# Kernel tuning notes

Measured on AMD Instinct MI355X. Metric: run time of the kernel, lower is better.

The kernel has to match this reference:

```python
import jax, jax.numpy as jnp
import numpy as np

HEADS = 8
DIM_HEAD = 32
SCALE = DIM_HEAD ** (-0.5)


def setup_inputs() -> dict:
    key = jax.random.key(0)
    k1, k2, k3, k4 = jax.random.split(key, 4)
    x = jax.random.normal(k1, (16, 256, 64, 64), dtype=jnp.float32)
    # conv 1x1 weights stored as [out_ch, in_ch]
    w_qkv = jax.random.normal(k2, (3 * HEADS * DIM_HEAD, 256), dtype=jnp.float32) * 0.05
    w_out = jax.random.normal(k3, (256, HEADS * DIM_HEAD), dtype=jnp.float32) * 0.05
    b_out = jax.random.normal(k4, (256,), dtype=jnp.float32) * 0.05
    return {"x": x, "w_qkv": w_qkv, "w_out": w_out, "b_out": b_out}


def reference(x, w_qkv, w_out, b_out):
    b, c, h, w = x.shape
    n = h * w
    # 1x1 conv (no bias) == channel matmul
    qkv = jnp.einsum('bchw,oc->bohw', x, w_qkv)            # [b, 3*H*D, h, w]
    qkv = qkv.reshape(b, 3, HEADS, DIM_HEAD, n)            # chunk then 'b (h c) xy'
    q, k, v = qkv[:, 0], qkv[:, 1], qkv[:, 2]              # [b, H, D, n]
    q = jax.nn.softmax(q, axis=-2) * SCALE                 # softmax over channel dim d
    k = jax.nn.softmax(k, axis=-1)                         # softmax over spatial n
    context = jnp.einsum('bhdn,bhen->bhde', k, v)          # [b, H, D, D]
    out = jnp.einsum('bhde,bhdn->bhen', context, q)        # [b, H, D, n]
    out = out.reshape(b, HEADS * DIM_HEAD, h, w)
    # 1x1 conv with bias
    return jnp.einsum('bchw,oc->bohw', out, w_out) + b_out[None, :, None, None]
```

## Files before the change

### kernel.cpp

```cpp
#include <hip/hip_runtime.h>
#include <cstddef>
#include <cstdint>

#define NN 4096
#define CIN 256
#define CQKV 768
#define NBATCH 16
#define KSPLIT 4
#define QSCALE 0.17677669529663687f

typedef short s16x8 __attribute__((ext_vector_type(8)));
typedef float f32x4 __attribute__((ext_vector_type(4)));

__device__ __forceinline__ float bf2f(unsigned short u) {
    unsigned int x = ((unsigned int)u) << 16;
    return __builtin_bit_cast(float, x);
}
__device__ __forceinline__ unsigned short f2bf(float f) {
    unsigned int u = __builtin_bit_cast(unsigned int, f);
    return (unsigned short)((u + 0x7fffu + ((u >> 16) & 1u)) >> 16);
}
__device__ __forceinline__ void glds16(const void* gsrc, void* lds) {
    __builtin_amdgcn_global_load_lds(
        (const __attribute__((address_space(1))) unsigned int*)gsrc,
        (__attribute__((address_space(3))) unsigned int*)lds,
        16, 0, 0);
}

__device__ __forceinline__ void gemm_core(const unsigned short* __restrict__ Ab,
                                          const unsigned short* __restrict__ Bb,
                                          int m0, int n0, char* smem,
                                          f32x4 (&acc)[4][4])
{
    const int t = threadIdx.x;
    const int lane = t & 63, w = t >> 6;
    const int lr = lane & 15, lq = lane >> 4;
    const int wr = (w >> 1) * 64, wc = (w & 1) * 64;
    const int srow = t >> 3;
    const int schunk = (t & 7) ^ (srow & 7);
    const int wq = w << 10;
    const int xr = lr & 7;

    char* A0 = smem;          char* B0 = smem + 16384;
    char* A1 = smem + 32768;  char* B1 = smem + 49152;

#define STG(bufA, bufB, k0)                                                     \
    { _Pragma("unroll") for (int i = 0; i < 4; ++i)                             \
        glds16(Ab + (size_t)(m0 + i*32 + srow)*256 + (k0) + schunk*8,           \
               (bufA) + i*4096 + wq);                                           \
      _Pragma("unroll") for (int i = 0; i < 4; ++i)                             \
        glds16(Bb + (size_t)(n0 + i*32 + srow)*256 + (k0) + schunk*8,           \
               (bufB) + i*4096 + wq); }

#define CMP(bufA, bufB)                                                         \
    { s16x8 af[4][2], bfr[4][2];                                                \
      _Pragma("unroll") for (int m = 0; m < 4; ++m) {                           \
        const char* rp = (bufA) + (wr + m*16 + lr)*128;                         \
        af[m][0] = *(const s16x8*)(rp + (((0*4 + lq) ^ xr) << 4));              \
        af[m][1] = *(const s16x8*)(rp + (((1*4 + lq) ^ xr) << 4)); }            \
      _Pragma("unroll") for (int n = 0; n < 4; ++n) {                           \
        const char* rp = (bufB) + (wc + n*16 + lr)*128;                         \
        bfr[n][0] = *(const s16x8*)(rp + (((0*4 + lq) ^ xr) << 4));             \
        bfr[n][1] = *(const s16x8*)(rp + (((1*4 + lq) ^ xr) << 4)); }           \
      _Pragma("unroll") for (int m = 0; m < 4; ++m)                             \
      _Pragma("unroll") for (int n = 0; n < 4; ++n) {                           \
        acc[m][n] = __builtin_amdgcn_mfma_f32_16x16x32_bf16(af[m][0], bfr[n][0], acc[m][n], 0, 0, 0); \
        acc[m][n] = __builtin_amdgcn_mfma_f32_16x16x32_bf16(af[m][1], bfr[n][1], acc[m][n], 0, 0, 0); }}

    STG(A0, B0, 0);
    __syncthreads();
    STG(A1, B1, 64);
    CMP(A0, B0);
    __syncthreads();
    STG(A0, B0, 128);
    CMP(A1, B1);
    __syncthreads();
    STG(A1, B1, 192);
    CMP(A0, B0);
    __syncthreads();
    CMP(A1, B1);
#undef STG
#undef CMP
}

__global__ __launch_bounds__(256, 2)
void gemm_qkv(const unsigned short* __restrict__ wb,
              const unsigned short* __restrict__ xT,
              unsigned short* __restrict__ qkv,
              unsigned short* __restrict__ qT)
{
    __shared__ __align__(16) char smem[65536];
    const int bz = blockIdx.z;
    const int m0 = blockIdx.y * 128, n0 = blockIdx.x * 128;
    const unsigned short* Bb = xT + (size_t)bz * NN * 256;

    f32x4 acc[4][4] = {};
    gemm_core(wb, Bb, m0, n0, smem, acc);

    const int t = threadIdx.x;
    const int lane = t & 63, w = t >> 6;
    const int lr = lane & 15, lq = lane >> 4;
    const int wr = (w >> 1) * 64, wc = (w & 1) * 64;

    if (m0 < 256) {
        __syncthreads();
        unsigned short (*qs)[136] = (unsigned short (*)[136])smem;
#pragma unroll
        for (int n = 0; n < 4; ++n) {
            const int col = wc + n * 16 + lr;
#pragma unroll
            for (int hp = 0; hp < 2; ++hp) {
                float mx = -1e30f;
#pragma unroll
                for (int u = 0; u < 2; ++u)
#pragma unroll
                    for (int r = 0; r < 4; ++r)
                        mx = fmaxf(mx, acc[hp * 2 + u][n][r]);
                mx = fmaxf(mx, __shfl_xor(mx, 16));
                mx = fmaxf(mx, __shfl_xor(mx, 32));
                float er[2][4];
                float s = 0.f;
#pragma unroll
                for (int u = 0; u < 2; ++u)
#pragma unroll
                    for (int r = 0; r < 4; ++r) {
                        er[u][r] = __expf(acc[hp * 2 + u][n][r] - mx);
                        s += er[u][r];
                    }
                s += __shfl_xor(s, 16);
                s += __shfl_xor(s, 32);
                const float inv = QSCALE / s;
#pragma unroll
                for (int u = 0; u < 2; ++u) {
                    ushort4 pk;
                    pk.x = f2bf(er[u][0] * inv);
                    pk.y = f2bf(er[u][1] * inv);
                    pk.z = f2bf(er[u][2] * inv);
                    pk.w = f2bf(er[u][3] * inv);
                    *(ushort4*)&qs[col][wr + (hp * 2 + u) * 16 + lq * 4] = pk;
                }
            }
        }
        __syncthreads();
        const int nl = t >> 1, half = t & 1;
        const unsigned short* src = &qs[nl][half * 64];
        unsigned short* dst = qT + ((size_t)bz * NN + n0 + nl) * 256 + m0 + half * 64;
#pragma unroll
        for (int i = 0; i < 8; ++i)
            *(s16x8*)(dst + i * 8) = *(const s16x8*)(src + i * 8);
    } else {
        unsigned short* Yb = qkv + (size_t)bz * CQKV * NN;
#pragma unroll
        for (int m = 0; m < 4; ++m)
#pragma unroll
            for (int r = 0; r < 4; ++r) {
                const int row = m0 + wr + m * 16 + lq * 4 + r;
#pragma unroll
                for (int n = 0; n < 4; ++n)
                    Yb[(size_t)row * NN + n0 + wc + n * 16 + lr] = f2bf(acc[m][n][r]);
            }
    }
}

__global__ __launch_bounds__(256, 2)
void gemm_out(const unsigned short* __restrict__ Mmat,
              const unsigned short* __restrict__ qT,
              float* __restrict__ out, const float* __restrict__ bias)
{
    __shared__ __align__(16) char smem[65536];
    const int bz = blockIdx.z;
    const int m0 = blockIdx.y * 128, n0 = blockIdx.x * 128;
    const unsigned short* Ab = Mmat + (size_t)bz * 256 * 256;
    const unsigned short* Bb = qT + (size_t)bz * NN * 256;

    f32x4 acc[4][4] = {};
    gemm_core(Ab, Bb, m0, n0, smem, acc);

    const int t = threadIdx.x;
    const int lane = t & 63, w = t >> 6;
    const int lr = lane & 15, lq = lane >> 4;
    const int wr = (w >> 1) * 64, wc = (w & 1) * 64;

    float* Yb = out + (size_t)bz * CIN * NN;
#pragma unroll
    for (int m = 0; m < 4; ++m)
#pragma unroll
        for (int r = 0; r < 4; ++r) {
            const int row = m0 + wr + m * 16 + lq * 4 + r;
            const float bv = bias[row];
#pragma unroll
            for (int n = 0; n < 4; ++n)
                Yb[(size_t)row * NN + n0 + wc + n * 16 + lr] = acc[m][n][r] + bv;
        }
}

__global__ __launch_bounds__(256)
void xpose(const float* __restrict__ x, unsigned short* __restrict__ xT)
{
    const int b = blockIdx.z;
    const int n0 = blockIdx.x * 64, c0 = blockIdx.y * 64;
    __shared__ float xs[64][65];
    const int t = threadIdx.x;
    const float* xb = x + (size_t)b * CIN * NN;
#pragma unroll
    for (int p = 0; p < 4; ++p) {
        const int row = p * 16 + (t >> 4);
        const int col = (t & 15) * 4;
        const float4 v = *reinterpret_cast<const float4*>(
            &xb[(size_t)(c0 + row) * NN + n0 + col]);
        xs[col + 0][row] = v.x; xs[col + 1][row] = v.y;
        xs[col + 2][row] = v.z; xs[col + 3][row] = v.w;
    }
    __syncthreads();
    const int n = t >> 2, cch = (t & 3) * 16;
    unsigned short arr[16];
#pragma unroll
    for (int e = 0; e < 16; ++e) arr[e] = f2bf(xs[n][cch + e]);
    unsigned short* dst = xT + ((size_t)b * NN + n0 + n) * 256 + c0 + cch;
    *reinterpret_cast<s16x8*>(&dst[0]) = *reinterpret_cast<s16x8*>(&arr[0]);
    *reinterpret_cast<s16x8*>(&dst[8]) = *reinterpret_cast<s16x8*>(&arr[8]);
}

__global__ __launch_bounds__(256)
void wcvt(const float* __restrict__ w, unsigned short* __restrict__ wb)
{
    const int i = (blockIdx.x * 256 + threadIdx.x) * 4;
    const float4 v = *reinterpret_cast<const float4*>(&w[i]);
    unsigned short a[4] = { f2bf(v.x), f2bf(v.y), f2bf(v.z), f2bf(v.w) };
    *reinterpret_cast<ushort2*>(&wb[i])     = *reinterpret_cast<ushort2*>(&a[0]);
    *reinterpret_cast<ushort2*>(&wb[i + 2]) = *reinterpret_cast<ushort2*>(&a[2]);
}

__global__ __launch_bounds__(256)
void kv_context(const unsigned short* __restrict__ qkv,
                float* __restrict__ ctx_part, float* __restrict__ z_part)
{
    const int bh = blockIdx.x;
    const int sp = blockIdx.y;
    const int b = bh >> 3, h = bh & 7;
    const unsigned short* kb = qkv + ((size_t)b * CQKV + 256 + h * 32) * NN;
    const unsigned short* vb = qkv + ((size_t)b * CQKV + 512 + h * 32) * NN;
    const int c0 = sp * (NN / KSPLIT);

    __shared__ float ek[64][36];
    __shared__ float vv[64][36];

    const int t = threadIdx.x;
    const int lane = t & 63;
    const int w = t >> 6;

    float zloc[8];
#pragma unroll
    for (int p = 0; p < 8; ++p) zloc[p] = 0.f;

    const int d0 = (lane >> 3) * 4;
    const int e0 = (lane & 7) * 4;
    float acc[4][4];
#pragma unroll
    for (int i = 0; i < 4; ++i)
#pragma unroll
        for (int j = 0; j < 4; ++j) acc[i][j] = 0.f;

    for (int cc = 0; cc < NN / KSPLIT; cc += 64) {
#pragma unroll
        for (int p = 0; p < 8; ++p) {
            const int d = w + 4 * p;
            const float kvv = bf2f(kb[(size_t)d * NN + c0 + cc + lane]);
            const float e = __expf(kvv);
            zloc[p] += e;
            ek[lane][d] = e;
            vv[lane][d] = bf2f(vb[(size_t)d * NN + c0 + cc + lane]);
        }
        __syncthreads();
#pragma unroll
        for (int ci = 0; ci < 16; ++ci) {
            const int c = w + 4 * ci;
            float ea[4], va[4];
            *reinterpret_cast<float4*>(ea) = *reinterpret_cast<const float4*>(&ek[c][d0]);
            *reinterpret_cast<float4*>(va) = *reinterpret_cast<const float4*>(&vv[c][e0]);
#pragma unroll
            for (int i = 0; i < 4; ++i)
#pragma unroll
                for (int j = 0; j < 4; ++j)
                    acc[i][j] = fmaf(ea[i], va[j], acc[i][j]);
        }
        __syncthreads();
    }

    float* dst = ctx_part + (((size_t)bh * KSPLIT + sp) * 4 + w) * 1024 + lane * 16;
#pragma unroll
    for (int i = 0; i < 4; ++i) {
        float4 v;
        v.x = acc[i][0]; v.y = acc[i][1]; v.z = acc[i][2]; v.w = acc[i][3];
        *reinterpret_cast<float4*>(&dst[i * 4]) = v;
    }
#pragma unroll
    for (int p = 0; p < 8; ++p) {
        float z = zloc[p];
#pragma unroll
        for (int off = 32; off >= 1; off >>= 1) z += __shfl_xor(z, off);
        if (lane == 0) z_part[((size_t)bh * KSPLIT + sp) * 32 + (w + 4 * p)] = z;
    }
}

__global__ __launch_bounds__(256)
void make_m(const float* __restrict__ ctx_part, const float* __restrict__ z_part,
            const float* __restrict__ w_out, unsigned short* __restrict__ Mmat)
{
    const int h = blockIdx.x;
    const int b = blockIdx.y;
    const int bh = b * 8 + h;
    const int t = threadIdx.x;

    __shared__ float ctx[32][33];
    __shared__ float zinv[32];

    for (int lin = t; lin < 1024; lin += 256) {
        const int g = lin >> 4, i = (lin >> 2) & 3, j = lin & 3;
        const int d = ((g >> 3) << 2) + i;
        const int e = ((g & 7) << 2) + j;
        float s = 0.f;
#pragma unroll
        for (int p = 0; p < 16; ++p)
            s += ctx_part[((size_t)bh * 16 + p) * 1024 + lin];
        ctx[d][e] = s;
    }
    if (t < 32) {
        float z = 0.f;
#pragma unroll
        for (int sp = 0; sp < KSPLIT; ++sp)
            z += z_part[((size_t)bh * KSPLIT + sp) * 32 + t];
        zinv[t] = 1.f / z;
    }
    __syncthreads();

    const int o = t;
    float wrow[32];
#pragma unroll
    for (int e = 0; e < 32; ++e)
        wrow[e] = w_out[(size_t)o * 256 + h * 32 + e];
#pragma unroll 4
    for (int d = 0; d < 32; ++d) {
        float s = 0.f;
#pragma unroll
        for (int e = 0; e < 32; ++e)
            s = fmaf(wrow[e], ctx[d][e], s);
        Mmat[((size_t)b * 256 + o) * 256 + h * 32 + d] = f2bf(s * zinv[d]);
    }
}

extern "C" void kernel_launch(void* const* d_in, const int* in_sizes, int n_in,
                              void* d_out, int out_size, void* d_ws, size_t ws_size,
                              hipStream_t stream)
{
    const float* x     = (const float*)d_in[0];
    const float* w_qkv = (const float*)d_in[1];
    const float* w_out = (const float*)d_in[2];
    const float* b_out = (const float*)d_in[3];
    float* out = (float*)d_out;

    char* ws = (char*)d_ws;
    size_t off = 0;
    unsigned short* qkv = (unsigned short*)(ws + off);  off += (size_t)NBATCH * CQKV * NN * 2;
    unsigned short* xT  = (unsigned short*)(ws + off);  off += (size_t)NBATCH * NN * CIN * 2;
    unsigned short* qT  = (unsigned short*)(ws + off);  off += (size_t)NBATCH * NN * CIN * 2;
    float* ctx_part     = (float*)(ws + off);           off += (size_t)128 * 16 * 1024 * 4;
    float* z_part       = (float*)(ws + off);           off += (size_t)128 * KSPLIT * 32 * 4;
    unsigned short* Mmat= (unsigned short*)(ws + off);  off += (size_t)NBATCH * 256 * 256 * 2;
    unsigned short* wb  = (unsigned short*)(ws + off);  off += (size_t)CQKV * CIN * 2;

    xpose<<<dim3(NN / 64, CIN / 64, NBATCH), 256, 0, stream>>>(x, xT);
    wcvt<<<dim3(CQKV * CIN / 1024), 256, 0, stream>>>(w_qkv, wb);

    gemm_qkv<<<dim3(32, 6, NBATCH), 256, 0, stream>>>(wb, xT, qkv, qT);

    kv_context<<<dim3(128, KSPLIT), 256, 0, stream>>>(qkv, ctx_part, z_part);

    make_m<<<dim3(8, NBATCH), 256, 0, stream>>>(ctx_part, z_part, w_out, Mmat);

    gemm_out<<<dim3(32, 2, NBATCH), 256, 0, stream>>>(Mmat, qT, out, b_out);
}
```

Measured before the change: 126.0 us.

## Fuse K/V projection with context accumulation into one QKV kernel

```diff
diff --git a/kernel.cpp b/kernel.cpp
--- a/kernel.cpp
+++ b/kernel.cpp
@@ -6,7 +6,6 @@
 #define CIN 256
 #define CQKV 768
 #define NBATCH 16
-#define KSPLIT 4
 #define QSCALE 0.17677669529663687f
 
 typedef short s16x8 __attribute__((ext_vector_type(8)));
@@ -27,10 +26,307 @@
         16, 0, 0);
 }
 
-__device__ __forceinline__ void gemm_core(const unsigned short* __restrict__ Ab,
-                                          const unsigned short* __restrict__ Bb,
-                                          int m0, int n0, char* smem,
-                                          f32x4 (&acc)[4][4])
+__global__ __launch_bounds__(256)
+void xpose(const float* __restrict__ x, unsigned short* __restrict__ xT)
+{
+    const int b = blockIdx.z;
+    const int n0 = blockIdx.x * 64, c0 = blockIdx.y * 64;
+    __shared__ float xs[64][65];
+    const int t = threadIdx.x;
+    const float* xb = x + (size_t)b * CIN * NN;
+#pragma unroll
+    for (int p = 0; p < 4; ++p) {
+        const int row = p * 16 + (t >> 4);
+        const int col = (t & 15) * 4;
+        const float4 v = *reinterpret_cast<const float4*>(
+            &xb[(size_t)(c0 + row) * NN + n0 + col]);
+        xs[col + 0][row] = v.x; xs[col + 1][row] = v.y;
+        xs[col + 2][row] = v.z; xs[col + 3][row] = v.w;
+    }
+    __syncthreads();
+    const int n = t >> 2, cch = (t & 3) * 16;
+    unsigned short arr[16];
+#pragma unroll
+    for (int e = 0; e < 16; ++e) arr[e] = f2bf(xs[n][cch + e]);
+    unsigned short* dst = xT + ((size_t)b * NN + n0 + n) * 256 + c0 + cch;
+    *reinterpret_cast<s16x8*>(&dst[0]) = *reinterpret_cast<s16x8*>(&arr[0]);
+    *reinterpret_cast<s16x8*>(&dst[8]) = *reinterpret_cast<s16x8*>(&arr[8]);
+}
+
+__global__ __launch_bounds__(256)
+void wcvt(const float* __restrict__ w, unsigned short* __restrict__ wb)
+{
+    const int i = (blockIdx.x * 256 + threadIdx.x) * 4;
+    const float4 v = *reinterpret_cast<const float4*>(&w[i]);
+    unsigned short a[4] = { f2bf(v.x), f2bf(v.y), f2bf(v.z), f2bf(v.w) };
+    *reinterpret_cast<ushort2*>(&wb[i])     = *reinterpret_cast<ushort2*>(&a[0]);
+    *reinterpret_cast<ushort2*>(&wb[i + 2]) = *reinterpret_cast<ushort2*>(&a[2]);
+}
+
+__device__ __forceinline__ void gemm32(const unsigned short* __restrict__ Ab,
+                                       const unsigned short* __restrict__ Bb,
+                                       char* __restrict__ smem, f32x4 (&acc)[4][4])
+{
+    const int t = threadIdx.x;
+    const int lane = t & 63, w = t >> 6;
+    const int lr = lane & 15, lq = lane >> 4;
+    const int wr = (w >> 1) * 64, wc = (w & 1) * 64;
+    const int srow = t >> 2;
+    const int schunk = (t & 3) ^ (srow & 3);
+    const int wq = w << 10;
+    const int slot = (lq ^ (lr & 3)) << 4;
+    char* A0 = smem;          char* B0 = smem + 8192;
+    char* A1 = smem + 16384;  char* B1 = smem + 24576;
+
+#define STG32(bufA, bufB, k0)                                                   \
+    { glds16(Ab + (size_t)(srow) * 256 + (k0) + schunk * 8, (bufA) + wq);       \
+      glds16(Ab + (size_t)(64 + srow) * 256 + (k0) + schunk * 8,                \
+             (bufA) + 4096 + wq);                                               \
+      glds16(Bb + (size_t)(srow) * 256 + (k0) + schunk * 8, (bufB) + wq);       \
+      glds16(Bb + (size_t)(64 + srow) * 256 + (k0) + schunk * 8,                \
+             (bufB) + 4096 + wq); }
+
+#define CMP32(bufA, bufB)                                                       \
+    { s16x8 af[4], bfr[4];                                                      \
+      _Pragma("unroll") for (int m = 0; m < 4; ++m)                             \
+        af[m] = *(const s16x8*)((bufA) + (wr + m * 16 + lr) * 64 + slot);       \
+      _Pragma("unroll") for (int n = 0; n < 4; ++n)                             \
+        bfr[n] = *(const s16x8*)((bufB) + (wc + n * 16 + lr) * 64 + slot);      \
+      _Pragma("unroll") for (int m = 0; m < 4; ++m)                             \
+      _Pragma("unroll") for (int n = 0; n < 4; ++n)                             \
+        acc[m][n] = __builtin_amdgcn_mfma_f32_16x16x32_bf16(af[m], bfr[n],      \
+                                                            acc[m][n], 0, 0, 0); }
+
+    STG32(A0, B0, 0);   __syncthreads();
+    STG32(A1, B1, 32);  CMP32(A0, B0); __syncthreads();
+    STG32(A0, B0, 64);  CMP32(A1, B1); __syncthreads();
+    STG32(A1, B1, 96);  CMP32(A0, B0); __syncthreads();
+    STG32(A0, B0, 128); CMP32(A1, B1); __syncthreads();
+    STG32(A1, B1, 160); CMP32(A0, B0); __syncthreads();
+    STG32(A0, B0, 192); CMP32(A1, B1); __syncthreads();
+    STG32(A1, B1, 224); CMP32(A0, B0); __syncthreads();
+    CMP32(A1, B1);
+#undef STG32
+#undef CMP32
+}
+
+__global__ __launch_bounds__(256, 2)
+void fused_qkv(const unsigned short* __restrict__ wb,
+               const unsigned short* __restrict__ xT,
+               unsigned short* __restrict__ qT,
+               float* __restrict__ ctx_part,
+               float* __restrict__ z_part)
+{
+    __shared__ __align__(16) char smem[49152];
+    const int nt = blockIdx.x, b = blockIdx.y;
+    const int n0 = nt * 128;
+    const unsigned short* Bb = xT + ((size_t)b * NN + n0) * 256;
+    const int t = threadIdx.x;
+    const int lane = t & 63, w = t >> 6;
+    const int lr = lane & 15, lq = lane >> 4;
+    const int wr = (w >> 1) * 64, wc = (w & 1) * 64;
+
+    f32x4 acc[4][4];
+    unsigned int ekpk[4][4][2];
+
+#pragma unroll
+    for (int mq = 0; mq < 2; ++mq) {
+#pragma unroll
+        for (int m = 0; m < 4; ++m)
+#pragma unroll
+            for (int n = 0; n < 4; ++n) acc[m][n] = (f32x4){0.f, 0.f, 0.f, 0.f};
+        gemm32(wb + (size_t)(mq * 128) * 256, Bb, smem, acc);
+        __syncthreads();
+        unsigned short (*qs)[136] = (unsigned short (*)[136])smem;
+#pragma unroll
+        for (int n = 0; n < 4; ++n) {
+            const int col = wc + n * 16 + lr;
+#pragma unroll
+            for (int hp = 0; hp < 2; ++hp) {
+                float mx = -1e30f;
+#pragma unroll
+                for (int u = 0; u < 2; ++u)
+#pragma unroll
+                    for (int r = 0; r < 4; ++r)
+                        mx = fmaxf(mx, acc[hp * 2 + u][n][r]);
+                mx = fmaxf(mx, __shfl_xor(mx, 16));
+                mx = fmaxf(mx, __shfl_xor(mx, 32));
+                float er[2][4];
+                float s = 0.f;
+#pragma unroll
+                for (int u = 0; u < 2; ++u)
+#pragma unroll
+                    for (int r = 0; r < 4; ++r) {
+                        er[u][r] = __expf(acc[hp * 2 + u][n][r] - mx);
+                        s += er[u][r];
+                    }
+                s += __shfl_xor(s, 16);
+                s += __shfl_xor(s, 32);
+                const float inv = QSCALE / s;
+#pragma unroll
+                for (int u = 0; u < 2; ++u) {
+                    ushort4 pk;
+                    pk.x = f2bf(er[u][0] * inv);
+                    pk.y = f2bf(er[u][1] * inv);
+                    pk.z = f2bf(er[u][2] * inv);
+                    pk.w = f2bf(er[u][3] * inv);
+                    *(ushort4*)&qs[col][wr + (hp * 2 + u) * 16 + lq * 4] = pk;
+                }
+            }
+        }
+        __syncthreads();
+        const int nl = t >> 1, half = t & 1;
+        const unsigned short* src = &qs[nl][half * 64];
+        unsigned short* dst = qT + ((size_t)b * NN + n0 + nl) * 256 + mq * 128 + half * 64;
+#pragma unroll
+        for (int i = 0; i < 8; ++i)
+            *(s16x8*)(dst + i * 8) = *(const s16x8*)(src + i * 8);
+        __syncthreads();
+    }
+
+#pragma unroll
+    for (int g = 0; g < 2; ++g) {
+#pragma unroll
+        for (int m = 0; m < 4; ++m)
+#pragma unroll
+            for (int n = 0; n < 4; ++n) acc[m][n] = (f32x4){0.f, 0.f, 0.f, 0.f};
+        gemm32(wb + (size_t)(256 + g * 128) * 256, Bb, smem, acc);
+
+        float zacc[4][4];
+#pragma unroll
+        for (int m = 0; m < 4; ++m)
+#pragma unroll
+            for (int r = 0; r < 4; ++r) zacc[m][r] = 0.f;
+#pragma unroll
+        for (int m = 0; m < 4; ++m)
+#pragma unroll
+            for (int n = 0; n < 4; ++n) {
+                const unsigned short u0 = f2bf(__expf(acc[m][n][0]));
+                const unsigned short u1 = f2bf(__expf(acc[m][n][1]));
+                const unsigned short u2 = f2bf(__expf(acc[m][n][2]));
+                const unsigned short u3 = f2bf(__expf(acc[m][n][3]));
+                zacc[m][0] += bf2f(u0);
+                zacc[m][1] += bf2f(u1);
+                zacc[m][2] += bf2f(u2);
+                zacc[m][3] += bf2f(u3);
+                ekpk[m][n][0] = (unsigned int)u0 | ((unsigned int)u1 << 16);
+                ekpk[m][n][1] = (unsigned int)u2 | ((unsigned int)u3 << 16);
+            }
+#pragma unroll
+        for (int m = 0; m < 4; ++m)
+#pragma unroll
+            for (int r = 0; r < 4; ++r) {
+                float z = zacc[m][r];
+                z += __shfl_xor(z, 1);
+                z += __shfl_xor(z, 2);
+                z += __shfl_xor(z, 4);
+                z += __shfl_xor(z, 8);
+                if (lr == 0)
+                    z_part[(((size_t)(b * 32 + nt)) * 2 + (wc >> 6)) * 256
+                           + g * 128 + wr + m * 16 + lq * 4 + r] = z;
+            }
+
+#pragma unroll
+        for (int m = 0; m < 4; ++m)
+#pragma unroll
+            for (int n = 0; n < 4; ++n) acc[m][n] = (f32x4){0.f, 0.f, 0.f, 0.f};
+        gemm32(wb + (size_t)(512 + g * 128) * 256, Bb, smem, acc);
+
+#pragma unroll
+        for (int hh = 0; hh < 4; ++hh) {
+            if (wr == (hh >> 1) * 64) {
+#pragma unroll
+                for (int mi = 0; mi < 2; ++mi) {
+                    const int m = ((hh & 1) << 1) + mi;
+                    const int drow = mi * 16 + lq * 4;
+#pragma unroll
+                    for (int n = 0; n < 4; ++n) {
+                        const int col = wc + n * 16 + lr;
+#pragma unroll
+                        for (int p = 0; p < 2; ++p) {
+                            const unsigned int wd = ekpk[m][n][p];
+                            const int d0 = drow + 2 * p, d1 = drow + 2 * p + 1;
+                            *(unsigned short*)(smem + 32768 +
+                                ((d0 * 256 + col * 2) ^ ((d0 & 7) << 4))) = (unsigned short)wd;
+                            *(unsigned short*)(smem + 32768 +
+                                ((d1 * 256 + col * 2) ^ ((d1 & 7) << 4))) = (unsigned short)(wd >> 16);
+                        }
+#pragma unroll
+                        for (int r = 0; r < 4; ++r) {
+                            const int e = drow + r;
+                            *(unsigned short*)(smem + 40960 +
+                                ((e * 256 + col * 2) ^ ((e & 7) << 4))) = f2bf(acc[m][n][r]);
+                        }
+                    }
+                }
+            }
+            __syncthreads();
+            const int fr = w >> 1, fc = w & 1;
+            f32x4 ca = {};
+#pragma unroll
+            for (int kc = 0; kc < 4; ++kc) {
+                const int ra = fr * 16 + lr, rb = fc * 16 + lr;
+                const s16x8 av = *(const s16x8*)(smem + 32768 +
+                    ((ra * 256 + kc * 64 + lq * 16) ^ ((ra & 7) << 4)));
+                const s16x8 bv = *(const s16x8*)(smem + 40960 +
+                    ((rb * 256 + kc * 64 + lq * 16) ^ ((rb & 7) << 4)));
+                ca = __builtin_amdgcn_mfma_f32_16x16x32_bf16(av, bv, ca, 0, 0, 0);
+            }
+            float* cp = ctx_part + (((size_t)(b * 32 + nt)) * 8 + g * 4 + hh) * 1024
+                        + (fr * 16 + lq * 4) * 32 + fc * 16 + lr;
+#pragma unroll
+            for (int r = 0; r < 4; ++r) cp[r * 32] = ca[r];
+            __syncthreads();
+        }
+    }
+}
+
+__global__ __launch_bounds__(256)
+void make_m(const float* __restrict__ ctx_part, const float* __restrict__ z_part,
+            const float* __restrict__ w_out, unsigned short* __restrict__ Mmat)
+{
+    const int h = blockIdx.x, b = blockIdx.y;
+    const int t = threadIdx.x;
+    __shared__ float ctx[32][33];
+    __shared__ float zinv[32];
+
+    for (int c = t; c < 1024; c += 256) {
+        float s = 0.f;
+#pragma unroll 8
+        for (int nt = 0; nt < 32; ++nt)
+            s += ctx_part[(((size_t)(b * 32 + nt)) * 8 + h) * 1024 + c];
+        ctx[c >> 5][c & 31] = s;
+    }
+    if (t < 32) {
+        float z = 0.f;
+#pragma unroll 8
+        for (int nt = 0; nt < 32; ++nt) {
+            z += z_part[(((size_t)(b * 32 + nt)) * 2 + 0) * 256 + h * 32 + t];
+            z += z_part[(((size_t)(b * 32 + nt)) * 2 + 1) * 256 + h * 32 + t];
+        }
+        zinv[t] = 1.f / z;
+    }
+    __syncthreads();
+
+    const int o = t;
+    float wrow[32];
+#pragma unroll
+    for (int e = 0; e < 32; ++e)
+        wrow[e] = w_out[(size_t)o * 256 + h * 32 + e];
+#pragma unroll 4
+    for (int d = 0; d < 32; ++d) {
+        float s = 0.f;
+#pragma unroll
+        for (int e = 0; e < 32; ++e)
+            s = fmaf(wrow[e], ctx[d][e], s);
+        Mmat[((size_t)b * 256 + o) * 256 + h * 32 + d] = f2bf(s * zinv[d]);
+    }
+}
+
+__device__ __forceinline__ void gemm_core64(const unsigned short* __restrict__ Ab,
+                                            const unsigned short* __restrict__ Bb,
+                                            int m0, int n0, char* smem,
+                                            f32x4 (&acc)[4][4])
 {
     const int t = threadIdx.x;
     const int lane = t & 63, w = t >> 6;
@@ -84,85 +380,6 @@
 }
 
 __global__ __launch_bounds__(256, 2)
-void gemm_qkv(const unsigned short* __restrict__ wb,
-              const unsigned short* __restrict__ xT,
-              unsigned short* __restrict__ qkv,
-              unsigned short* __restrict__ qT)
-{
-    __shared__ __align__(16) char smem[65536];
-    const int bz = blockIdx.z;
-    const int m0 = blockIdx.y * 128, n0 = blockIdx.x * 128;
-    const unsigned short* Bb = xT + (size_t)bz * NN * 256;
-
-    f32x4 acc[4][4] = {};
-    gemm_core(wb, Bb, m0, n0, smem, acc);
-
-    const int t = threadIdx.x;
-    const int lane = t & 63, w = t >> 6;
-    const int lr = lane & 15, lq = lane >> 4;
-    const int wr = (w >> 1) * 64, wc = (w & 1) * 64;
-
-    if (m0 < 256) {
-        __syncthreads();
-        unsigned short (*qs)[136] = (unsigned short (*)[136])smem;
-#pragma unroll
-        for (int n = 0; n < 4; ++n) {
-            const int col = wc + n * 16 + lr;
-#pragma unroll
-            for (int hp = 0; hp < 2; ++hp) {
-                float mx = -1e30f;
-#pragma unroll
-                for (int u = 0; u < 2; ++u)
-#pragma unroll
-                    for (int r = 0; r < 4; ++r)
-                        mx = fmaxf(mx, acc[hp * 2 + u][n][r]);
-                mx = fmaxf(mx, __shfl_xor(mx, 16));
-                mx = fmaxf(mx, __shfl_xor(mx, 32));
-                float er[2][4];
-                float s = 0.f;
-#pragma unroll
-                for (int u = 0; u < 2; ++u)
-#pragma unroll
-                    for (int r = 0; r < 4; ++r) {
-                        er[u][r] = __expf(acc[hp * 2 + u][n][r] - mx);
-                        s += er[u][r];
-                    }
-                s += __shfl_xor(s, 16);
-                s += __shfl_xor(s, 32);
-                const float inv = QSCALE / s;
-#pragma unroll
-                for (int u = 0; u < 2; ++u) {
-                    ushort4 pk;
-                    pk.x = f2bf(er[u][0] * inv);
-                    pk.y = f2bf(er[u][1] * inv);
-                    pk.z = f2bf(er[u][2] * inv);
-                    pk.w = f2bf(er[u][3] * inv);
-                    *(ushort4*)&qs[col][wr + (hp * 2 + u) * 16 + lq * 4] = pk;
-                }
-            }
-        }
-        __syncthreads();
-        const int nl = t >> 1, half = t & 1;
-        const unsigned short* src = &qs[nl][half * 64];
-        unsigned short* dst = qT + ((size_t)bz * NN + n0 + nl) * 256 + m0 + half * 64;
-#pragma unroll
-        for (int i = 0; i < 8; ++i)
-            *(s16x8*)(dst + i * 8) = *(const s16x8*)(src + i * 8);
-    } else {
-        unsigned short* Yb = qkv + (size_t)bz * CQKV * NN;
-#pragma unroll
-        for (int m = 0; m < 4; ++m)
-#pragma unroll
-            for (int r = 0; r < 4; ++r) {
-                const int row = m0 + wr + m * 16 + lq * 4 + r;
-#pragma unroll
-                for (int n = 0; n < 4; ++n)
-                    Yb[(size_t)row * NN + n0 + wc + n * 16 + lr] = f2bf(acc[m][n][r]);
-            }
-    }
-}
-
-__global__ __launch_bounds__(256, 2)
 void gemm_out(const unsigned short* __restrict__ Mmat,
               const unsigned short* __restrict__ qT,
               float* __restrict__ out, const float* __restrict__ bias)
@@ -174,7 +391,7 @@
     const unsigned short* Bb = qT + (size_t)bz * NN * 256;
 
     f32x4 acc[4][4] = {};
-    gemm_core(Ab, Bb, m0, n0, smem, acc);
+    gemm_core64(Ab, Bb, m0, n0, smem, acc);
 
     const int t = threadIdx.x;
     const int lane = t & 63, w = t >> 6;
@@ -192,161 +409,6 @@
             for (int n = 0; n < 4; ++n)
                 Yb[(size_t)row * NN + n0 + wc + n * 16 + lr] = acc[m][n][r] + bv;
         }
-}
-
-__global__ __launch_bounds__(256)
-void xpose(const float* __restrict__ x, unsigned short* __restrict__ xT)
-{
-    const int b = blockIdx.z;
-    const int n0 = blockIdx.x * 64, c0 = blockIdx.y * 64;
-    __shared__ float xs[64][65];
-    const int t = threadIdx.x;
-    const float* xb = x + (size_t)b * CIN * NN;
-#pragma unroll
-    for (int p = 0; p < 4; ++p) {
-        const int row = p * 16 + (t >> 4);
-        const int col = (t & 15) * 4;
-        const float4 v = *reinterpret_cast<const float4*>(
-            &xb[(size_t)(c0 + row) * NN + n0 + col]);
-        xs[col + 0][row] = v.x; xs[col + 1][row] = v.y;
-        xs[col + 2][row] = v.z; xs[col + 3][row] = v.w;
-    }
-    __syncthreads();
-    const int n = t >> 2, cch = (t & 3) * 16;
-    unsigned short arr[16];
-#pragma unroll
-    for (int e = 0; e < 16; ++e) arr[e] = f2bf(xs[n][cch + e]);
-    unsigned short* dst = xT + ((size_t)b * NN + n0 + n) * 256 + c0 + cch;
-    *reinterpret_cast<s16x8*>(&dst[0]) = *reinterpret_cast<s16x8*>(&arr[0]);
-    *reinterpret_cast<s16x8*>(&dst[8]) = *reinterpret_cast<s16x8*>(&arr[8]);
-}
-
-__global__ __launch_bounds__(256)
-void wcvt(const float* __restrict__ w, unsigned short* __restrict__ wb)
-{
-    const int i = (blockIdx.x * 256 + threadIdx.x) * 4;
-    const float4 v = *reinterpret_cast<const float4*>(&w[i]);
-    unsigned short a[4] = { f2bf(v.x), f2bf(v.y), f2bf(v.z), f2bf(v.w) };
-    *reinterpret_cast<ushort2*>(&wb[i])     = *reinterpret_cast<ushort2*>(&a[0]);
-    *reinterpret_cast<ushort2*>(&wb[i + 2]) = *reinterpret_cast<ushort2*>(&a[2]);
-}
-
-__global__ __launch_bounds__(256)
-void kv_context(const unsigned short* __restrict__ qkv,
-                float* __restrict__ ctx_part, float* __restrict__ z_part)
-{
-    const int bh = blockIdx.x;
-    const int sp = blockIdx.y;
-    const int b = bh >> 3, h = bh & 7;
-    const unsigned short* kb = qkv + ((size_t)b * CQKV + 256 + h * 32) * NN;
-    const unsigned short* vb = qkv + ((size_t)b * CQKV + 512 + h * 32) * NN;
-    const int c0 = sp * (NN / KSPLIT);
-
-    __shared__ float ek[64][36];
-    __shared__ float vv[64][36];
-
-    const int t = threadIdx.x;
-    const int lane = t & 63;
-    const int w = t >> 6;
-
-    float zloc[8];
-#pragma unroll
-    for (int p = 0; p < 8; ++p) zloc[p] = 0.f;
-
-    const int d0 = (lane >> 3) * 4;
-    const int e0 = (lane & 7) * 4;
-    float acc[4][4];
-#pragma unroll
-    for (int i = 0; i < 4; ++i)
-#pragma unroll
-        for (int j = 0; j < 4; ++j) acc[i][j] = 0.f;
-
-    for (int cc = 0; cc < NN / KSPLIT; cc += 64) {
-#pragma unroll
-        for (int p = 0; p < 8; ++p) {
-            const int d = w + 4 * p;
-            const float kvv = bf2f(kb[(size_t)d * NN + c0 + cc + lane]);
-            const float e = __expf(kvv);
-            zloc[p] += e;
-            ek[lane][d] = e;
-            vv[lane][d] = bf2f(vb[(size_t)d * NN + c0 + cc + lane]);
-        }
-        __syncthreads();
-#pragma unroll
-        for (int ci = 0; ci < 16; ++ci) {
-            const int c = w + 4 * ci;
-            float ea[4], va[4];
-            *reinterpret_cast<float4*>(ea) = *reinterpret_cast<const float4*>(&ek[c][d0]);
-            *reinterpret_cast<float4*>(va) = *reinterpret_cast<const float4*>(&vv[c][e0]);
-#pragma unroll
-            for (int i = 0; i < 4; ++i)
-#pragma unroll
-                for (int j = 0; j < 4; ++j)
-                    acc[i][j] = fmaf(ea[i], va[j], acc[i][j]);
-        }
-        __syncthreads();
-    }
-
-    float* dst = ctx_part + (((size_t)bh * KSPLIT + sp) * 4 + w) * 1024 + lane * 16;
-#pragma unroll
-    for (int i = 0; i < 4; ++i) {
-        float4 v;
-        v.x = acc[i][0]; v.y = acc[i][1]; v.z = acc[i][2]; v.w = acc[i][3];
-        *reinterpret_cast<float4*>(&dst[i * 4]) = v;
-    }
-#pragma unroll
-    for (int p = 0; p < 8; ++p) {
-        float z = zloc[p];
-#pragma unroll
-        for (int off = 32; off >= 1; off >>= 1) z += __shfl_xor(z, off);
-        if (lane == 0) z_part[((size_t)bh * KSPLIT + sp) * 32 + (w + 4 * p)] = z;
-    }
-}
-
-__global__ __launch_bounds__(256)
-void make_m(const float* __restrict__ ctx_part, const float* __restrict__ z_part,
-            const float* __restrict__ w_out, unsigned short* __restrict__ Mmat)
-{
-    const int h = blockIdx.x;
-    const int b = blockIdx.y;
-    const int bh = b * 8 + h;
-    const int t = threadIdx.x;
-
-    __shared__ float ctx[32][33];
-    __shared__ float zinv[32];
-
-    for (int lin = t; lin < 1024; lin += 256) {
-        const int g = lin >> 4, i = (lin >> 2) & 3, j = lin & 3;
-        const int d = ((g >> 3) << 2) + i;
-        const int e = ((g & 7) << 2) + j;
-        float s = 0.f;
-#pragma unroll
-        for (int p = 0; p < 16; ++p)
-            s += ctx_part[((size_t)bh * 16 + p) * 1024 + lin];
-        ctx[d][e] = s;
-    }
-    if (t < 32) {
-        float z = 0.f;
-#pragma unroll
-        for (int sp = 0; sp < KSPLIT; ++sp)
-            z += z_part[((size_t)bh * KSPLIT + sp) * 32 + t];
-        zinv[t] = 1.f / z;
-    }
-    __syncthreads();
-
-    const int o = t;
-    float wrow[32];
-#pragma unroll
-    for (int e = 0; e < 32; ++e)
-        wrow[e] = w_out[(size_t)o * 256 + h * 32 + e];
-#pragma unroll 4
-    for (int d = 0; d < 32; ++d) {
-        float s = 0.f;
-#pragma unroll
-        for (int e = 0; e < 32; ++e)
-            s = fmaf(wrow[e], ctx[d][e], s);
-        Mmat[((size_t)b * 256 + o) * 256 + h * 32 + d] = f2bf(s * zinv[d]);
-    }
 }
 
 extern "C" void kernel_launch(void* const* d_in, const int* in_sizes, int n_in,
@@ -361,20 +423,17 @@
 
     char* ws = (char*)d_ws;
     size_t off = 0;
-    unsigned short* qkv = (unsigned short*)(ws + off);  off += (size_t)NBATCH * CQKV * NN * 2;
     unsigned short* xT  = (unsigned short*)(ws + off);  off += (size_t)NBATCH * NN * CIN * 2;
     unsigned short* qT  = (unsigned short*)(ws + off);  off += (size_t)NBATCH * NN * CIN * 2;
-    float* ctx_part     = (float*)(ws + off);           off += (size_t)128 * 16 * 1024 * 4;
-    float* z_part       = (float*)(ws + off);           off += (size_t)128 * KSPLIT * 32 * 4;
+    float* ctx_part     = (float*)(ws + off);           off += (size_t)NBATCH * 32 * 8 * 1024 * 4;
+    float* z_part       = (float*)(ws + off);           off += (size_t)NBATCH * 32 * 2 * 256 * 4;
     unsigned short* Mmat= (unsigned short*)(ws + off);  off += (size_t)NBATCH * 256 * 256 * 2;
     unsigned short* wb  = (unsigned short*)(ws + off);  off += (size_t)CQKV * CIN * 2;
 
     xpose<<<dim3(NN / 64, CIN / 64, NBATCH), 256, 0, stream>>>(x, xT);
     wcvt<<<dim3(CQKV * CIN / 1024), 256, 0, stream>>>(w_qkv, wb);
 
-    gemm_qkv<<<dim3(32, 6, NBATCH), 256, 0, stream>>>(wb, xT, qkv, qT);
-
-    kv_context<<<dim3(128, KSPLIT), 256, 0, stream>>>(qkv, ctx_part, z_part);
+    fused_qkv<<<dim3(32, NBATCH), 256, 0, stream>>>(wb, xT, qT, ctx_part, z_part);
 
     make_m<<<dim3(8, NBATCH), 256, 0, stream>>>(ctx_part, z_part, w_out, Mmat);
 
```

New measurement: 131.4 us. 1.04x slower.
